# Kernel optimization log

Measured on AMD Instinct MI355X. Metric: run time of the kernel, lower is better.

The kernel has to match this reference:

```python
import jax, jax.numpy as jnp
import numpy as np

B, T, I, H, O = 4096, 256, 5, 64, 25


def _lstm_layer(x, Wih, Whh, bih, bhh):
    """One LSTM layer, batch_first. x: [B,T,in], Wih: [4H,in], Whh: [4H,H].
    PyTorch gate order: i, f, g, o."""
    b, t, _ = x.shape
    h_dim = Whh.shape[1]
    # Precompute input contribution for all timesteps: [B,T,4H]
    gx = jnp.einsum('bti,gi->btg', x, Wih) + bih + bhh

    def step(carry, g_t):
        h, c = carry
        gates = g_t + h @ Whh.T  # [B,4H]
        i, f, g, o = jnp.split(gates, 4, axis=-1)
        i = jax.nn.sigmoid(i)
        f = jax.nn.sigmoid(f)
        g = jnp.tanh(g)
        o = jax.nn.sigmoid(o)
        c = f * c + i * g
        h = o * jnp.tanh(c)
        return (h, c), h

    h0 = jnp.zeros((b, h_dim), x.dtype)
    (_, _), hs = jax.lax.scan(step, (h0, h0), jnp.swapaxes(gx, 0, 1))  # hs: [T,B,H]
    return jnp.swapaxes(hs, 0, 1)  # [B,T,H]


def setup_inputs() -> dict:
    key = jax.random.key(0)
    ks = jax.random.split(key, 12)
    k = 1.0 / np.sqrt(H)  # torch LSTM/Linear init scale
    u = lambda kk, shp: jax.random.uniform(kk, shp, jnp.float32, -k, k)
    return {
        'x': jax.random.normal(ks[0], (B, T, I), jnp.float32),
        'Wih0': u(ks[1], (4 * H, I)),
        'Whh0': u(ks[2], (4 * H, H)),
        'bih0': u(ks[3], (4 * H,)),
        'bhh0': u(ks[4], (4 * H,)),
        'Wih1': u(ks[5], (4 * H, H)),
        'Whh1': u(ks[6], (4 * H, H)),
        'bih1': u(ks[7], (4 * H,)),
        'bhh1': u(ks[8], (4 * H,)),
        'Wfc': u(ks[9], (O, H)),
        'bfc': u(ks[10], (O,)),
    }


def reference(x, Wih0, Whh0, bih0, bhh0, Wih1, Whh1, bih1, bhh1, Wfc, bfc):
    # 2-layer LSTM (dropout = identity in eval mode)
    h1 = _lstm_layer(x, Wih0, Whh0, bih0, bhh0)   # [B,T,H]
    h2 = _lstm_layer(h1, Wih1, Whh1, bih1, bhh1)  # [B,T,H]
    last = h2[:, -1, :]                            # [B,H]
    out = last @ Wfc.T + bfc                       # [B,25]
    return out.reshape(x.shape[0], 5, 5)
```

## Files before the change

kernel.cpp:

```cpp
#include <hip/hip_runtime.h>


#define TT   256
#define II   5
#define HH   64
#define OO   25
#define MT   16
#define NTHR 1024
#define XP   520
#define HSZ  1024
#define HF   65

typedef __attribute__((ext_vector_type(8))) short  short8;
typedef __attribute__((ext_vector_type(4))) float  floatx4;

#define MFMA(a, b, c) __builtin_amdgcn_mfma_f32_16x16x32_bf16(a, b, c, 0, 0, 0)

__device__ __forceinline__ float frcp(float x) { return __builtin_amdgcn_rcpf(x); }
__device__ __forceinline__ float fsig(float x) {
    return frcp(1.f + __builtin_amdgcn_exp2f(x * -1.44269504f));
}
__device__ __forceinline__ float ftanhf(float x) {
    return 1.f - 2.f * frcp(1.f + __builtin_amdgcn_exp2f(x * 2.88539008f));
}
__device__ __forceinline__ unsigned short bf16_rne(float f) {
    unsigned int u = __builtin_bit_cast(unsigned int, f);
    u += 0x7FFFu + ((u >> 16) & 1u);
    return (unsigned short)(u >> 16);
}
__device__ __forceinline__ float cell_update(const floatx4& g, float& c) {
    const float gi = fsig  (g[0]);
    const float gf = fsig  (g[1]);
    const float gz = ftanhf(g[2]);
    const float go = fsig  (g[3]);
    c = gf * c + gi * gz;
    return go * ftanhf(c);
}

__global__ __attribute__((amdgpu_flat_work_group_size(1024, 1024),
                          amdgpu_waves_per_eu(4, 4)))
void lstm_mfma8(const float* __restrict__ x,
                const float* __restrict__ Wih0, const float* __restrict__ Whh0,
                const float* __restrict__ bih0, const float* __restrict__ bhh0,
                const float* __restrict__ Wih1, const float* __restrict__ Whh1,
                const float* __restrict__ bih1, const float* __restrict__ bhh1,
                const float* __restrict__ Wfc,  const float* __restrict__ bfc,
                float* __restrict__ out)
{
    __shared__ __align__(16) unsigned short xhi[MT * XP];
    __shared__ __align__(16) unsigned short h1hi[2 * HSZ];
    __shared__ __align__(16) unsigned short h2hi[2 * HSZ];
    __shared__ __align__(16) float          h2f[MT * HF];

    const int tid   = threadIdx.x;
    const int w     = tid >> 6;
    const int lane  = tid & 63;
    const int b     = lane & 15;
    const int q     = lane >> 4;
    const int jmine = 4 * w + q;
    const int hw_off = ((jmine >> 3) * 16 + b) * 8 + (jmine & 7);
    const int ro     = lane * 8;

    short8 A1h[2];
    short8 A2h[4];
    short8 Axwh;
    {
        const int rr = lane & 15;
        const int g  = (rr & 3) * 64 + 4 * w + (rr >> 2);
        #pragma unroll
        for (int c = 0; c < 2; ++c)
            #pragma unroll
            for (int jj = 0; jj < 8; ++jj)
                A1h[c][jj] = (short)bf16_rne(Whh0[g * HH + c * 32 + q * 8 + jj]);
        #pragma unroll
        for (int c = 0; c < 4; ++c)
            #pragma unroll
            for (int jj = 0; jj < 8; ++jj) {
                const int k = c * 32 + q * 8 + jj;
                float wv = (k < HH) ? Wih1[g * HH + k] : Whh1[g * HH + (k - HH)];
                A2h[c][jj] = (short)bf16_rne(wv);
            }
        #pragma unroll
        for (int jj = 0; jj < 8; ++jj) {
            const int k = q * 8 + jj;
            Axwh[jj] = (k < II) ? (short)bf16_rne(Wih0[g * II + k]) : (short)0;
        }
    }
    float bias1[4], bias2[4];
    #pragma unroll
    for (int r = 0; r < 4; ++r) {
        const int g = r * 64 + jmine;
        bias1[r] = bih0[g] + bhh0[g];
        bias2[r] = bih1[g] + bhh1[g];
    }

    for (int i = tid; i < MT * XP / 2; i += NTHR)
        ((unsigned int*)xhi)[i] = 0u;
    for (int i = tid; i < HSZ; i += NTHR) {
        ((unsigned int*)h1hi)[i] = 0u;
        ((unsigned int*)h2hi)[i] = 0u;
    }
    float c1 = 0.f, c2 = 0.f;
    __syncthreads();

    const int blockBase = blockIdx.x * MT;

    auto refill_x = [&](int t0) {
        const int rb = tid >> 6, dt = tid & 63;
        const float* src = x + ((size_t)(blockBase + rb) * TT + t0 + dt) * II;
        unsigned short* ph = xhi + rb * XP + dt * 8;
        #pragma unroll
        for (int ii = 0; ii < II; ++ii)
            ph[ii] = bf16_rne(src[ii]);
    };

    refill_x(0);
    __syncthreads();
    {
        short8 Bxh = *(const short8*)(xhi + b * XP);
        floatx4 a1 = {bias1[0], bias1[1], bias1[2], bias1[3]};
        a1 = MFMA(Axwh, Bxh, a1);
        const float h = cell_update(a1, c1);
        h1hi[0 * HSZ + hw_off] = bf16_rne(h);
    }
    __syncthreads();

    for (int i = 0; i < TT - 1; ++i) {
        if (((i + 1) & 63) == 0) {
            refill_x(i + 1);
            __syncthreads();
        }
        const int wp = i & 1, rp = wp ^ 1;
        const int dt = (i + 1) & 63;

        short8 H1h0 = *(const short8*)(h1hi + wp * HSZ + ro);
        short8 H1h1 = *(const short8*)(h1hi + wp * HSZ + 512 + ro);
        short8 H2h0 = *(const short8*)(h2hi + rp * HSZ + ro);
        short8 H2h1 = *(const short8*)(h2hi + rp * HSZ + 512 + ro);
        short8 Bxh  = *(const short8*)(xhi + b * XP + dt * 8);

        floatx4 a2 = {bias2[0], bias2[1], bias2[2], bias2[3]};
        a2 = MFMA(A2h[0], H1h0, a2);
        a2 = MFMA(A2h[1], H1h1, a2);
        a2 = MFMA(A2h[2], H2h0, a2);
        a2 = MFMA(A2h[3], H2h1, a2);

        floatx4 a1 = {bias1[0], bias1[1], bias1[2], bias1[3]};
        a1 = MFMA(Axwh, Bxh, a1);
        a1 = MFMA(A1h[0], H1h0, a1);
        a1 = MFMA(A1h[1], H1h1, a1);

        {
            const float h = cell_update(a2, c2);
            h2hi[wp * HSZ + hw_off] = bf16_rne(h);
        }
        {
            const float h = cell_update(a1, c1);
            h1hi[rp * HSZ + hw_off] = bf16_rne(h);
        }
        __syncthreads();
    }

    {
        const int wp = 1, rp = 0;
        short8 H1h0 = *(const short8*)(h1hi + wp * HSZ + ro);
        short8 H1h1 = *(const short8*)(h1hi + wp * HSZ + 512 + ro);
        short8 H2h0 = *(const short8*)(h2hi + rp * HSZ + ro);
        short8 H2h1 = *(const short8*)(h2hi + rp * HSZ + 512 + ro);
        floatx4 a2 = {bias2[0], bias2[1], bias2[2], bias2[3]};
        a2 = MFMA(A2h[0], H1h0, a2);
        a2 = MFMA(A2h[1], H1h1, a2);
        a2 = MFMA(A2h[2], H2h0, a2);
        a2 = MFMA(A2h[3], H2h1, a2);
        const float h = cell_update(a2, c2);
        h2f[b * HF + jmine] = h;
    }
    __syncthreads();

    if (tid < MT * OO) {
        const int bb = tid / OO, o = tid - bb * OO;
        float acc = bfc[o];
        const float* wr = Wfc + o * HH;
        const float* hr = h2f + bb * HF;
        #pragma unroll
        for (int j = 0; j < HH; ++j) acc += wr[j] * hr[j];
        out[((size_t)blockIdx.x * MT + bb) * OO + o] = acc;
    }
}

extern "C" void kernel_launch(void* const* d_in, const int* in_sizes, int n_in,
                              void* d_out, int out_size, void* d_ws, size_t ws_size,
                              hipStream_t stream) {
    const float* x    = (const float*)d_in[0];
    const float* Wih0 = (const float*)d_in[1];
    const float* Whh0 = (const float*)d_in[2];
    const float* bih0 = (const float*)d_in[3];
    const float* bhh0 = (const float*)d_in[4];
    const float* Wih1 = (const float*)d_in[5];
    const float* Whh1 = (const float*)d_in[6];
    const float* bih1 = (const float*)d_in[7];
    const float* bhh1 = (const float*)d_in[8];
    const float* Wfc  = (const float*)d_in[9];
    const float* bfc  = (const float*)d_in[10];
    float* out = (float*)d_out;

    dim3 grid(4096 / MT), block(NTHR);
    lstm_mfma8<<<grid, block, 0, stream>>>(x, Wih0, Whh0, bih0, bhh0,
                                           Wih1, Whh1, bih1, bhh1,
                                           Wfc, bfc, out);
}
```

Baseline: 283.1 us.

## Fold activation exp2 scales into weights and unroll timestep loop by two

Pre-multiplies the recurrent and input weights and biases by the log2e-based scale factors (-log2e for sigmoid gates, 2·log2e for the tanh gate), so the cell update skips one multiply per gate and uses fma for the tanh and cell combine. It also unrolls the time loop by two so the ping-pong buffer indices become constants, and walks the x buffer with a pointer instead of recomputing the offset. Scaling the weights before bf16 rounding changes rounding slightly, which may affect accuracy.

```diff
diff --git a/kernel.cpp b/kernel.cpp
--- a/kernel.cpp
+++ b/kernel.cpp
@@ -17,29 +17,25 @@
 #define MFMA(a, b, c) __builtin_amdgcn_mfma_f32_16x16x32_bf16(a, b, c, 0, 0, 0)
 
 __device__ __forceinline__ float frcp(float x) { return __builtin_amdgcn_rcpf(x); }
-__device__ __forceinline__ float fsig(float x) {
-    return frcp(1.f + __builtin_amdgcn_exp2f(x * -1.44269504f));
-}
-__device__ __forceinline__ float ftanhf(float x) {
-    return 1.f - 2.f * frcp(1.f + __builtin_amdgcn_exp2f(x * 2.88539008f));
-}
+__device__ __forceinline__ float fexp2(float x) { return __builtin_amdgcn_exp2f(x); }
 __device__ __forceinline__ unsigned short bf16_rne(float f) {
     unsigned int u = __builtin_bit_cast(unsigned int, f);
     u += 0x7FFFu + ((u >> 16) & 1u);
     return (unsigned short)(u >> 16);
 }
 __device__ __forceinline__ float cell_update(const floatx4& g, float& c) {
-    const float gi = fsig  (g[0]);
-    const float gf = fsig  (g[1]);
-    const float gz = ftanhf(g[2]);
-    const float go = fsig  (g[3]);
-    c = gf * c + gi * gz;
-    return go * ftanhf(c);
+    const float gi = frcp(1.f + fexp2(g[0]));
+    const float gf = frcp(1.f + fexp2(g[1]));
+    const float gz = fmaf(-2.f, frcp(1.f + fexp2(g[2])), 1.f);
+    const float go = frcp(1.f + fexp2(g[3]));
+    c = fmaf(gf, c, gi * gz);
+    const float tc = fmaf(-2.f, frcp(1.f + fexp2(c * 2.885390082f)), 1.f);
+    return go * tc;
 }
 
 __global__ __attribute__((amdgpu_flat_work_group_size(1024, 1024),
                           amdgpu_waves_per_eu(4, 4)))
-void lstm_mfma8(const float* __restrict__ x,
+void lstm_mfma9(const float* __restrict__ x,
                 const float* __restrict__ Wih0, const float* __restrict__ Whh0,
                 const float* __restrict__ bih0, const float* __restrict__ bhh0,
                 const float* __restrict__ Wih1, const float* __restrict__ Whh1,
@@ -67,31 +63,33 @@
     {
         const int rr = lane & 15;
         const int g  = (rr & 3) * 64 + 4 * w + (rr >> 2);
+        const float sc = ((rr & 3) == 2) ? 2.885390082f : -1.442695041f;
         #pragma unroll
         for (int c = 0; c < 2; ++c)
             #pragma unroll
             for (int jj = 0; jj < 8; ++jj)
-                A1h[c][jj] = (short)bf16_rne(Whh0[g * HH + c * 32 + q * 8 + jj]);
+                A1h[c][jj] = (short)bf16_rne(sc * Whh0[g * HH + c * 32 + q * 8 + jj]);
         #pragma unroll
         for (int c = 0; c < 4; ++c)
             #pragma unroll
             for (int jj = 0; jj < 8; ++jj) {
                 const int k = c * 32 + q * 8 + jj;
                 float wv = (k < HH) ? Wih1[g * HH + k] : Whh1[g * HH + (k - HH)];
-                A2h[c][jj] = (short)bf16_rne(wv);
+                A2h[c][jj] = (short)bf16_rne(sc * wv);
             }
         #pragma unroll
         for (int jj = 0; jj < 8; ++jj) {
             const int k = q * 8 + jj;
-            Axwh[jj] = (k < II) ? (short)bf16_rne(Wih0[g * II + k]) : (short)0;
+            Axwh[jj] = (k < II) ? (short)bf16_rne(sc * Wih0[g * II + k]) : (short)0;
         }
     }
     float bias1[4], bias2[4];
     #pragma unroll
     for (int r = 0; r < 4; ++r) {
         const int g = r * 64 + jmine;
-        bias1[r] = bih0[g] + bhh0[g];
-        bias2[r] = bih1[g] + bhh1[g];
+        const float sc = (r == 2) ? 2.885390082f : -1.442695041f;
+        bias1[r] = sc * (bih0[g] + bhh0[g]);
+        bias2[r] = sc * (bih1[g] + bhh1[g]);
     }
 
     for (int i = tid; i < MT * XP / 2; i += NTHR)
@@ -125,48 +123,53 @@
     }
     __syncthreads();
 
-    for (int i = 0; i < TT - 1; ++i) {
-        if (((i + 1) & 63) == 0) {
-            refill_x(i + 1);
+    const unsigned short* xptr = xhi + b * XP + 8;
+
+#define STEP_BODY(WP, RP)                                                     \
+    {                                                                         \
+        short8 H1h0 = *(const short8*)(h1hi + (WP) * HSZ + ro);               \
+        short8 H1h1 = *(const short8*)(h1hi + (WP) * HSZ + 512 + ro);         \
+        short8 H2h0 = *(const short8*)(h2hi + (RP) * HSZ + ro);               \
+        short8 H2h1 = *(const short8*)(h2hi + (RP) * HSZ + 512 + ro);         \
+        short8 Bxh  = *(const short8*)(xptr);                                 \
+        xptr += 8;                                                            \
+        floatx4 a2 = {bias2[0], bias2[1], bias2[2], bias2[3]};                \
+        a2 = MFMA(A2h[0], H1h0, a2);                                          \
+        a2 = MFMA(A2h[1], H1h1, a2);                                          \
+        a2 = MFMA(A2h[2], H2h0, a2);                                          \
+        a2 = MFMA(A2h[3], H2h1, a2);                                          \
+        floatx4 a1 = {bias1[0], bias1[1], bias1[2], bias1[3]};                \
+        a1 = MFMA(Axwh, Bxh, a1);                                             \
+        a1 = MFMA(A1h[0], H1h0, a1);                                          \
+        a1 = MFMA(A1h[1], H1h1, a1);                                          \
+        {                                                                     \
+            const float h = cell_update(a2, c2);                              \
+            h2hi[(WP) * HSZ + hw_off] = bf16_rne(h);                          \
+        }                                                                     \
+        {                                                                     \
+            const float h = cell_update(a1, c1);                              \
+            h1hi[(RP) * HSZ + hw_off] = bf16_rne(h);                          \
+        }                                                                     \
+        __syncthreads();                                                      \
+    }
+
+    for (int i = 0; i < 254; i += 2) {
+        STEP_BODY(0, 1)
+        if (((i + 2) & 63) == 0) {
+            refill_x(i + 2);
+            xptr = xhi + b * XP;
             __syncthreads();
         }
-        const int wp = i & 1, rp = wp ^ 1;
-        const int dt = (i + 1) & 63;
-
-        short8 H1h0 = *(const short8*)(h1hi + wp * HSZ + ro);
-        short8 H1h1 = *(const short8*)(h1hi + wp * HSZ + 512 + ro);
-        short8 H2h0 = *(const short8*)(h2hi + rp * HSZ + ro);
-        short8 H2h1 = *(const short8*)(h2hi + rp * HSZ + 512 + ro);
-        short8 Bxh  = *(const short8*)(xhi + b * XP + dt * 8);
-
-        floatx4 a2 = {bias2[0], bias2[1], bias2[2], bias2[3]};
-        a2 = MFMA(A2h[0], H1h0, a2);
-        a2 = MFMA(A2h[1], H1h1, a2);
-        a2 = MFMA(A2h[2], H2h0, a2);
-        a2 = MFMA(A2h[3], H2h1, a2);
-
-        floatx4 a1 = {bias1[0], bias1[1], bias1[2], bias1[3]};
-        a1 = MFMA(Axwh, Bxh, a1);
-        a1 = MFMA(A1h[0], H1h0, a1);
-        a1 = MFMA(A1h[1], H1h1, a1);
-
-        {
-            const float h = cell_update(a2, c2);
-            h2hi[wp * HSZ + hw_off] = bf16_rne(h);
-        }
-        {
-            const float h = cell_update(a1, c1);
-            h1hi[rp * HSZ + hw_off] = bf16_rne(h);
-        }
-        __syncthreads();
-    }
+        STEP_BODY(1, 0)
+    }
+    STEP_BODY(0, 1)
+#undef STEP_BODY
 
     {
-        const int wp = 1, rp = 0;
-        short8 H1h0 = *(const short8*)(h1hi + wp * HSZ + ro);
-        short8 H1h1 = *(const short8*)(h1hi + wp * HSZ + 512 + ro);
-        short8 H2h0 = *(const short8*)(h2hi + rp * HSZ + ro);
-        short8 H2h1 = *(const short8*)(h2hi + rp * HSZ + 512 + ro);
+        short8 H1h0 = *(const short8*)(h1hi + 1 * HSZ + ro);
+        short8 H1h1 = *(const short8*)(h1hi + 1 * HSZ + 512 + ro);
+        short8 H2h0 = *(const short8*)(h2hi + 0 * HSZ + ro);
+        short8 H2h1 = *(const short8*)(h2hi + 0 * HSZ + 512 + ro);
         floatx4 a2 = {bias2[0], bias2[1], bias2[2], bias2[3]};
         a2 = MFMA(A2h[0], H1h0, a2);
         a2 = MFMA(A2h[1], H1h1, a2);
@@ -205,7 +208,7 @@
     float* out = (float*)d_out;
 
     dim3 grid(4096 / MT), block(NTHR);
-    lstm_mfma8<<<grid, block, 0, stream>>>(x, Wih0, Whh0, bih0, bhh0,
+    lstm_mfma9<<<grid, block, 0, stream>>>(x, Wih0, Whh0, bih0, bhh0,
                                            Wih1, Whh1, bih1, bhh1,
                                            Wfc, bfc, out);
 }
```

Result: faster. 259.7 us (-8.2%).
